# Kernel tuning notes

Measured on AMD Instinct MI355X. Metric: run time of the kernel, lower is better.

Reference implementation:

```python
import jax, jax.numpy as jnp
import numpy as np

B, S, H, I, NH, E = 16, 512, 1024, 4096, 16, 8
DH = H // NH
EPS = 1e-12


def layer_norm(x, g, b):
    mu = jnp.mean(x, axis=-1, keepdims=True)
    var = jnp.mean(jnp.square(x - mu), axis=-1, keepdims=True)
    return (x - mu) * jax.lax.rsqrt(var + EPS) * g + b


def setup_inputs() -> dict:
    key = jax.random.key(0)
    ks = jax.random.split(key, 16)
    s_h = 1.0 / np.sqrt(H)
    s_i = 1.0 / np.sqrt(I)
    return {
        "hidden_states": jax.random.normal(ks[0], (B, S, H), jnp.float32),
        "Wq": jax.random.normal(ks[1], (H, H), jnp.float32) * s_h,
        "bq": jnp.zeros((H,), jnp.float32),
        "Wk": jax.random.normal(ks[2], (H, H), jnp.float32) * s_h,
        "bk": jnp.zeros((H,), jnp.float32),
        "Wv": jax.random.normal(ks[3], (H, H), jnp.float32) * s_h,
        "bv": jnp.zeros((H,), jnp.float32),
        "Wo": jax.random.normal(ks[4], (H, H), jnp.float32) * s_h,
        "bo": jnp.zeros((H,), jnp.float32),
        "ln1_g": jnp.ones((H,), jnp.float32),
        "ln1_b": jnp.zeros((H,), jnp.float32),
        "ln2_g": jnp.ones((H,), jnp.float32),
        "ln2_b": jnp.zeros((H,), jnp.float32),
        "gate_W": jax.random.normal(ks[5], (H, E), jnp.float32) * s_h,
        "W_up": jax.random.normal(ks[6], (E, H, I), jnp.float32) * s_h,
        "b_up": jnp.zeros((E, I), jnp.float32),
        "W_down": jax.random.normal(ks[7], (E, I, H), jnp.float32) * s_i,
        "b_down": jnp.zeros((E, H), jnp.float32),
    }


def reference(hidden_states, Wq, bq, Wk, bk, Wv, bv, Wo, bo,
              ln1_g, ln1_b, ln2_g, ln2_b, gate_W, W_up, b_up, W_down, b_down):
    x = hidden_states
    # --- BERT self-attention ---
    q = (x @ Wq + bq).reshape(B, S, NH, DH)
    k = (x @ Wk + bk).reshape(B, S, NH, DH)
    v = (x @ Wv + bv).reshape(B, S, NH, DH)
    scores = jnp.einsum("bqhd,bkhd->bhqk", q, k) / np.sqrt(DH)
    probs = jax.nn.softmax(scores, axis=-1)
    ctx = jnp.einsum("bhqk,bkhd->bqhd", probs, v).reshape(B, S, H)
    # BertSelfOutput: dense + residual + LayerNorm
    attn_out = layer_norm(ctx @ Wo + bo + x, ln1_g, ln1_b)

    # --- feed_forward_chunk: pre-LN, MoE, residual (residual on attn_out) ---
    x_ln = layer_norm(attn_out, ln2_g, ln2_b)
    router_output = jnp.einsum("bsh,he->bse", x_ln, gate_W)
    router_logits = jnp.mean(router_output, axis=1)          # [B, E]
    choice = jnp.argmax(router_logits, axis=-1)              # softmax-argmax == logits-argmax

    # per-sample top-1 expert: gather each sample's expert weights, batched GEMM
    Wu = W_up[choice]                                        # [B, H, I]
    Wd = W_down[choice]                                      # [B, I, H]
    h = jax.nn.gelu(jnp.einsum("bsh,bhi->bsi", x_ln, Wu) + b_up[choice][:, None, :],
                    approximate=False)
    moe = jnp.einsum("bsi,bih->bsh", h, Wd) + b_down[choice][:, None, :]
    layer_output = moe + attn_out
    return (layer_output, router_logits)
```

## Files before the change

### kernel.cpp

```cpp
#include <hip/hip_runtime.h>


typedef __attribute__((ext_vector_type(4))) float f32x4;
typedef __attribute__((ext_vector_type(8))) short s8v;
typedef __attribute__((ext_vector_type(4))) short s4v;
typedef unsigned short u16;

#define DEV static __device__ __forceinline__

DEV u16 f2bf(float f){
  union { float f; unsigned u; } v; v.f = f;
  unsigned r = v.u + 0x7fffu + ((v.u >> 16) & 1u);
  return (u16)(r >> 16);
}

DEV f32x4 mfma16(s8v a, s8v b, f32x4 c){
  return __builtin_amdgcn_mfma_f32_16x16x32_bf16(a, b, c, 0, 0, 0);
}

DEV float wave_sum(float s){
#pragma unroll
  for (int o = 1; o < 64; o <<= 1) s += __shfl_xor(s, o);
  return s;
}

#define ASYNC_COPY16(g, l) \
  __builtin_amdgcn_global_load_lds((const __attribute__((address_space(1))) void*)(g), \
                                   (__attribute__((address_space(3))) void*)(l), 16, 0, 0)

__global__ __launch_bounds__(256) void cvt_bf16(const float* __restrict__ in,
                                                u16* __restrict__ out)
{
  const size_t i = ((size_t)blockIdx.x * 256 + threadIdx.x) * 8;
  f32x4 a = *(const f32x4*)&in[i];
  f32x4 b = *(const f32x4*)&in[i + 4];
  s8v o;
#pragma unroll
  for (int j = 0; j < 4; ++j){ o[j] = (short)f2bf(a[j]); o[4 + j] = (short)f2bf(b[j]); }
  *(s8v*)&out[i] = o;
}

__global__ __launch_bounds__(256) void transpose_w(const float* __restrict__ in,
                                                   u16* __restrict__ out, int R, int C)
{
  __shared__ float t[64][65];
  const size_t bs = (size_t)blockIdx.z * R * (size_t)C;
  in += bs; out += bs;
  const int c0 = blockIdx.x * 64, r0 = blockIdx.y * 64;
  const int tx = threadIdx.x & 63, ty = threadIdx.x >> 6;
#pragma unroll
  for (int j = 0; j < 64; j += 4) t[ty + j][tx] = in[(size_t)(r0 + ty + j) * C + c0 + tx];
  __syncthreads();
#pragma unroll
  for (int j = 0; j < 64; j += 4) out[(size_t)(c0 + ty + j) * R + r0 + tx] = f2bf(t[tx][ty + j]);
}

template<int MODE, bool SWZ>
__global__ __launch_bounds__(256, 2) void gemm_bt(
    const u16* __restrict__ A, const u16* __restrict__ Bt,
    const float* __restrict__ bias, void* __restrict__ outp,
    const float* __restrict__ resid, int M, int N, int K,
    const int* __restrict__ choice,
    long aBatch, long outBatch, long residBatch, long btExpert, long biasExpert,
    void* __restrict__ out2, void* __restrict__ out3)
{
  int bx, by, bz;
  if (SWZ){
    const int nx = gridDim.x, ny = gridDim.y;
    const int nwg = nx * ny * gridDim.z;
    int id = blockIdx.x + nx * (blockIdx.y + ny * blockIdx.z);
    if ((nwg & 7) == 0){ const int q = nwg >> 3; id = (id & 7) * q + (id >> 3); }
    bx = id % nx; const int r2 = id / nx; by = r2 % ny; bz = r2 / ny;
  } else {
    bx = blockIdx.x; by = blockIdx.y; bz = blockIdx.z;
  }
  const int z = bz;
  if (choice){
    const int e = choice[z];
    Bt   += (size_t)e * btExpert;
    bias += (size_t)e * biasExpert;
  }
  A += (size_t)z * aBatch;

  const int tid = threadIdx.x;
  const int lane = tid & 63, wid = tid >> 6;
  const int hi = lane >> 4, l15 = lane & 15;
  const int wr = wid >> 1, wc = wid & 1;
  const long row0 = (long)bx * 128;
  const long col0 = (long)by * 128;

  __shared__ __align__(16) u16 lA[3][128 * 32];
  __shared__ __align__(16) u16 lB[3][128 * 32];

  f32x4 acc[4][4];
#pragma unroll
  for (int i = 0; i < 4; ++i)
#pragma unroll
    for (int j = 0; j < 4; ++j) acc[i][j] = f32x4{0.f, 0.f, 0.f, 0.f};

  const int r0 = tid >> 2;
  const int scol = (((tid & 3) ^ ((tid >> 3) & 3)) << 3);
  const u16* pA[2]; const u16* pB[2];
#pragma unroll
  for (int j = 0; j < 2; ++j){
    pA[j] = A  + (row0 + j * 64 + r0) * (size_t)K + scol;
    pB[j] = Bt + (col0 + j * 64 + r0) * (size_t)K + scol;
  }

#define GSTAGE(S_) do { \
  _Pragma("unroll") \
  for (int j = 0; j < 2; ++j) ASYNC_COPY16(pA[j], &lA[S_][(j * 256 + tid) * 8]); \
  _Pragma("unroll") \
  for (int j = 0; j < 2; ++j) ASYNC_COPY16(pB[j], &lB[S_][(j * 256 + tid) * 8]); \
  _Pragma("unroll") \
  for (int j = 0; j < 2; ++j){ pA[j] += 32; pB[j] += 32; } \
} while (0)

  const int rkey = (l15 >> 1) & 3;
  const int baseA = (wr * 64 + l15) * 32 + ((hi ^ rkey) << 3);
  const int baseB = (wc * 64 + l15) * 32 + ((hi ^ rkey) << 3);

#define ITER(S_, S2_, WSTR_, DOSTAGE_) do { \
  asm volatile("s_waitcnt vmcnt(" WSTR_ ")" ::: "memory"); \
  __builtin_amdgcn_s_barrier(); \
  __builtin_amdgcn_sched_barrier(0); \
  if (DOSTAGE_) GSTAGE(S2_); \
  s8v af[4], bfv[4]; \
  _Pragma("unroll") \
  for (int mi = 0; mi < 4; ++mi) af[mi] = *(const s8v*)&lA[S_][baseA + mi * 512]; \
  _Pragma("unroll") \
  for (int ni = 0; ni < 4; ++ni) bfv[ni] = *(const s8v*)&lB[S_][baseB + ni * 512]; \
  __builtin_amdgcn_s_setprio(1); \
  _Pragma("unroll") \
  for (int mi = 0; mi < 4; ++mi) \
    _Pragma("unroll") \
    for (int ni = 0; ni < 4; ++ni) \
      acc[mi][ni] = mfma16(af[mi], bfv[ni], acc[mi][ni]); \
  __builtin_amdgcn_s_setprio(0); \
} while (0)

  const int nk = K >> 5;
  GSTAGE(0); GSTAGE(1);

  for (int t = 0; t < nk - 2; t += 3){
    ITER(0, 2, "4", 1);
    ITER(1, 0, "4", 1);
    ITER(2, 1, "4", 1);
  }
  ITER(0, 0, "4", 0);
  ITER(1, 0, "0", 0);
#undef ITER
#undef GSTAGE

#pragma unroll
  for (int mi = 0; mi < 4; ++mi){
    const long rowb = row0 + wr * 64 + mi * 16 + hi * 4;
#pragma unroll
    for (int ni = 0; ni < 4; ++ni){
      const long col = col0 + wc * 64 + ni * 16 + l15;
      const float bv = bias[col];
#pragma unroll
      for (int r = 0; r < 4; ++r){
        const long row = rowb + r;
        float v = acc[mi][ni][r] + bv;
        if (MODE == 2){
          float* o = (float*)outp + (size_t)z * outBatch;
          const float* rs = resid + (size_t)z * residBatch;
          o[row * N + col] = v + rs[row * N + col];
        } else if (MODE == 1){
          u16* o = (u16*)outp + (size_t)z * outBatch;
          const float gv = 0.5f * v * (1.0f + erff(v * 0.70710678118654752f));
          o[row * N + col] = f2bf(gv);
        } else if (MODE == 4){
          const int seg = (int)(col >> 10), lc = (int)(col & 1023);
          const u16 bv16 = f2bf(v);
          if (seg == 0)      ((u16*)outp)[row * 1024 + lc] = bv16;
          else if (seg == 1) ((u16*)out2)[row * 1024 + lc] = bv16;
          else {
            const int bb = (int)(row >> 9), ss = (int)(row & 511);
            const int hh = lc >> 6, dd = lc & 63;
            ((u16*)out3)[(((size_t)(bb * 16 + hh)) * 64 + dd) * 512 + ss] = bv16;
          }
        }
      }
    }
  }
}

__global__ __launch_bounds__(256) void attn_fwd(
    const u16* __restrict__ qb, const u16* __restrict__ kb,
    const u16* __restrict__ vt, u16* __restrict__ ctx)
{
  const int tid = threadIdx.x;
  const int lane = tid & 63, wid = tid >> 6;
  const int hi = lane >> 4, l15 = lane & 15;
  const int h = blockIdx.y, b = blockIdx.z;
  const int q0 = blockIdx.x * 128 + wid * 32;

  const u16* kp0 = kb + (size_t)b * 512 * 1024 + h * 64;
  const u16* vp0 = vt + ((size_t)(b * 16 + h)) * 64 * 512;

  __shared__ __align__(16) u16 lK[2][64 * 64];
  __shared__ __align__(16) u16 lV[2][64 * 64];
  __shared__ __align__(16) u16 lP[4][2][16][72];

#define STAGE(bsel, k0s) do { \
  _Pragma("unroll") \
  for (int i = 0; i < 2; ++i){ \
    const int idx = i * 256 + tid; \
    const int row = idx >> 3, seg = idx & 7; \
    const int sc = ((seg ^ (row & 7)) << 3); \
    ASYNC_COPY16(kp0 + (size_t)((k0s) + row) * 1024 + sc, &lK[bsel][idx * 8]); \
    ASYNC_COPY16(vp0 + (size_t)row * 512 + (k0s) + sc,    &lV[bsel][idx * 8]); \
  } \
} while (0)

  const u16* qp = qb + ((size_t)b * 512 + q0) * 1024 + h * 64;
  s8v qf[2][2];
#pragma unroll
  for (int qt = 0; qt < 2; ++qt)
#pragma unroll
    for (int st = 0; st < 2; ++st)
      qf[qt][st] = *(const s8v*)&qp[(size_t)(qt * 16 + l15) * 1024 + st * 32 + hi * 8];

  f32x4 o[2][4];
#pragma unroll
  for (int qt = 0; qt < 2; ++qt)
#pragma unroll
    for (int mi = 0; mi < 4; ++mi) o[qt][mi] = f32x4{0.f, 0.f, 0.f, 0.f};
  float mrun[2] = {-3e38f, -3e38f}, lrun[2] = {0.f, 0.f};

  STAGE(0, 0);
  __syncthreads();

  for (int t = 0; t < 8; ++t){
    const int buf = t & 1;
    if (t < 7) STAGE(buf ^ 1, (t + 1) * 64);

    f32x4 s[2][4];
#pragma unroll
    for (int qt = 0; qt < 2; ++qt)
#pragma unroll
      for (int kt = 0; kt < 4; ++kt) s[qt][kt] = f32x4{0.f, 0.f, 0.f, 0.f};
#pragma unroll
    for (int st = 0; st < 2; ++st){
      s8v kf[4];
#pragma unroll
      for (int kt = 0; kt < 4; ++kt){
        const int row = kt * 16 + l15;
        kf[kt] = *(const s8v*)&lK[buf][row * 64 + (((st * 4 + hi) ^ (row & 7)) << 3)];
      }
#pragma unroll
      for (int qt = 0; qt < 2; ++qt)
#pragma unroll
        for (int kt = 0; kt < 4; ++kt)
          s[qt][kt] = mfma16(kf[kt], qf[qt][st], s[qt][kt]);
    }

#pragma unroll
    for (int qt = 0; qt < 2; ++qt){
      float mx = s[qt][0][0];
#pragma unroll
      for (int kt = 0; kt < 4; ++kt)
#pragma unroll
        for (int r = 0; r < 4; ++r) mx = fmaxf(mx, s[qt][kt][r]);
      mx *= 0.125f;
      mx = fmaxf(mx, __shfl_xor(mx, 16));
      mx = fmaxf(mx, __shfl_xor(mx, 32));
      const float mnew = fmaxf(mrun[qt], mx);
      const float alpha = __expf(mrun[qt] - mnew);
      mrun[qt] = mnew;
      float ps = 0.f;
#pragma unroll
      for (int kt = 0; kt < 4; ++kt){
        s4v pk;
#pragma unroll
        for (int r = 0; r < 4; ++r){
          const float p = __expf(s[qt][kt][r] * 0.125f - mnew);
          ps += p; pk[r] = (short)f2bf(p);
        }
        *(s4v*)&lP[wid][qt][l15][kt * 16 + 4 * hi] = pk;
      }
      ps += __shfl_xor(ps, 16);
      ps += __shfl_xor(ps, 32);
      lrun[qt] = lrun[qt] * alpha + ps;
#pragma unroll
      for (int mi = 0; mi < 4; ++mi)
#pragma unroll
        for (int r = 0; r < 4; ++r) o[qt][mi][r] *= alpha;
    }

#pragma unroll
    for (int ks = 0; ks < 2; ++ks){
      s8v vf[4];
#pragma unroll
      for (int mi = 0; mi < 4; ++mi){
        const int row = mi * 16 + l15;
        vf[mi] = *(const s8v*)&lV[buf][row * 64 + (((ks * 4 + hi) ^ (row & 7)) << 3)];
      }
#pragma unroll
      for (int qt = 0; qt < 2; ++qt){
        const s8v pf = *(const s8v*)&lP[wid][qt][l15][ks * 32 + 8 * hi];
#pragma unroll
        for (int mi = 0; mi < 4; ++mi)
          o[qt][mi] = mfma16(vf[mi], pf, o[qt][mi]);
      }
    }
    __syncthreads();
  }
#undef STAGE

#pragma unroll
  for (int qt = 0; qt < 2; ++qt){
    const float inv = 1.f / lrun[qt];
    u16* cp = ctx + ((size_t)b * 512 + q0 + qt * 16 + l15) * 1024 + h * 64;
#pragma unroll
    for (int mi = 0; mi < 4; ++mi)
#pragma unroll
      for (int r = 0; r < 4; ++r)
        cp[mi * 16 + 4 * hi + r] = f2bf(o[qt][mi][r] * inv);
  }
}

__global__ __launch_bounds__(256, 2) void ln12_colsum(
    float* __restrict__ t, const float* __restrict__ g1, const float* __restrict__ b1,
    const float* __restrict__ g2, const float* __restrict__ b2,
    u16* __restrict__ xln, float* __restrict__ colsum)
{
  const int b = blockIdx.y;
  const int wid = threadIdx.x >> 6, lane = threadIdx.x & 63;
  __shared__ float cacc[1024];
  for (int i = threadIdx.x; i < 1024; i += 256) cacc[i] = 0.f;
  __syncthreads();
  float acc[16];
#pragma unroll
  for (int i = 0; i < 16; ++i) acc[i] = 0.f;
  const int rbase = b * 512 + blockIdx.x * 64 + wid * 16;
  for (int rr = 0; rr < 16; ++rr){
    float* p = t + (size_t)(rbase + rr) * 1024;
    f32x4 v[4];
#pragma unroll
    for (int c = 0; c < 4; ++c) v[c] = *(const f32x4*)&p[c * 256 + lane * 4];
    float s = 0.f;
#pragma unroll
    for (int c = 0; c < 4; ++c) s += v[c][0] + v[c][1] + v[c][2] + v[c][3];
    const float mu = wave_sum(s) * (1.f / 1024.f);
    float s2 = 0.f;
#pragma unroll
    for (int c = 0; c < 4; ++c)
#pragma unroll
      for (int j = 0; j < 4; ++j){ const float d = v[c][j] - mu; s2 += d * d; }
    const float rs = rsqrtf(wave_sum(s2) * (1.f / 1024.f) + 1e-12f);
    float y1s = 0.f;
#pragma unroll
    for (int c = 0; c < 4; ++c){
      const f32x4 gg = *(const f32x4*)&g1[c * 256 + lane * 4];
      const f32x4 bb = *(const f32x4*)&b1[c * 256 + lane * 4];
#pragma unroll
      for (int j = 0; j < 4; ++j){
        v[c][j] = (v[c][j] - mu) * rs * gg[j] + bb[j];
        y1s += v[c][j];
      }
      *(f32x4*)&p[c * 256 + lane * 4] = v[c];
    }
    const float mu2 = wave_sum(y1s) * (1.f / 1024.f);
    float s22 = 0.f;
#pragma unroll
    for (int c = 0; c < 4; ++c)
#pragma unroll
      for (int j = 0; j < 4; ++j){ const float d = v[c][j] - mu2; s22 += d * d; }
    const float rs2 = rsqrtf(wave_sum(s22) * (1.f / 1024.f) + 1e-12f);
    u16* op = xln + (size_t)(rbase + rr) * 1024;
#pragma unroll
    for (int c = 0; c < 4; ++c){
      const f32x4 gg = *(const f32x4*)&g2[c * 256 + lane * 4];
      const f32x4 bb = *(const f32x4*)&b2[c * 256 + lane * 4];
      s4v ov;
#pragma unroll
      for (int j = 0; j < 4; ++j){
        const float y = (v[c][j] - mu2) * rs2 * gg[j] + bb[j];
        acc[c * 4 + j] += y;
        ov[j] = (short)f2bf(y);
      }
      *(s4v*)&op[c * 256 + lane * 4] = ov;
    }
  }
#pragma unroll
  for (int c = 0; c < 4; ++c)
#pragma unroll
    for (int j = 0; j < 4; ++j)
      atomicAdd(&cacc[c * 256 + lane * 4 + j], acc[c * 4 + j]);
  __syncthreads();
  for (int i = threadIdx.x; i < 1024; i += 256) atomicAdd(&colsum[b * 1024 + i], cacc[i]);
}

__global__ void router_argmax(const float* __restrict__ colsum, const float* __restrict__ gate,
                              float* __restrict__ logits, int* __restrict__ choice)
{
  const int b = blockIdx.x, lane = threadIdx.x;
  float pa[8];
#pragma unroll
  for (int e = 0; e < 8; ++e) pa[e] = 0.f;
  for (int it = 0; it < 16; ++it){
    const int hh = it * 64 + lane;
    const float c = colsum[b * 1024 + hh];
    const float* gp = gate + (size_t)hh * 8;
#pragma unroll
    for (int e = 0; e < 8; ++e) pa[e] += c * gp[e];
  }
#pragma unroll
  for (int e = 0; e < 8; ++e) pa[e] = wave_sum(pa[e]);
  if (lane == 0){
    float best = -3e38f; int bi = 0;
#pragma unroll
    for (int e = 0; e < 8; ++e){
      const float lg = pa[e] * (1.f / 512.f);
      logits[b * 8 + e] = lg;
      if (lg > best){ best = lg; bi = e; }
    }
    choice[b] = bi;
  }
}

extern "C" void kernel_launch(void* const* d_in, const int* in_sizes, int n_in,
                              void* d_out, int out_size, void* d_ws, size_t ws_size,
                              hipStream_t stream)
{
  const float* x    = (const float*)d_in[0];
  const float* Wq   = (const float*)d_in[1];
  const float* bq   = (const float*)d_in[2];
  const float* Wk   = (const float*)d_in[3];
  const float* bk   = (const float*)d_in[4];
  const float* Wv   = (const float*)d_in[5];
  const float* bv   = (const float*)d_in[6];
  const float* Wo   = (const float*)d_in[7];
  const float* bo   = (const float*)d_in[8];
  const float* ln1g = (const float*)d_in[9];
  const float* ln1b = (const float*)d_in[10];
  const float* ln2g = (const float*)d_in[11];
  const float* ln2b = (const float*)d_in[12];
  const float* gate = (const float*)d_in[13];
  const float* Wup  = (const float*)d_in[14];
  const float* bup  = (const float*)d_in[15];
  const float* Wdn  = (const float*)d_in[16];
  const float* bdn  = (const float*)d_in[17];

  size_t off = 0;
  char* wsb = (char*)d_ws;
  auto take = [&](size_t n) -> void* {
    void* p = wsb + off; off += (n + 255) & ~(size_t)255; return p;
  };
  u16*   x_bf  = (u16*)take(8192ull * 1024 * 2);
  u16*   Wqt   = (u16*)take(1024ull * 1024 * 2);
  u16*   Wkt   = (u16*)take(1024ull * 1024 * 2);
  u16*   Wvt   = (u16*)take(1024ull * 1024 * 2);
  u16*   Wot   = (u16*)take(1024ull * 1024 * 2);
  u16*   q_bf  = (u16*)take(8192ull * 1024 * 2);
  u16*   k_bf  = (u16*)take(8192ull * 1024 * 2);
  u16*   vt_bf = (u16*)take(8192ull * 1024 * 2);
  float* tmp   = (float*)take(8192ull * 1024 * 4);
  u16*   Wupt  = (u16*)take(8ull * 4096 * 1024 * 2);
  u16*   Wdnt  = (u16*)take(8ull * 1024 * 4096 * 2);
  u16*   h_bf  = (u16*)take(8192ull * 4096 * 2);
  float* colsum = (float*)take(16ull * 1024 * 4);
  int*   choice = (int*)take(256);
  float* qkvb  = (float*)take(3072 * 4);

  u16* ctx = x_bf;
  u16* xln = q_bf;
  float* logits = (float*)d_out + 8388608;

  cvt_bf16<<<4096, 256, 0, stream>>>(x, x_bf);
  transpose_w<<<dim3(16, 16, 1), 256, 0, stream>>>(Wq,  Wqt,  1024, 1024);
  transpose_w<<<dim3(16, 16, 1), 256, 0, stream>>>(Wk,  Wkt,  1024, 1024);
  transpose_w<<<dim3(16, 16, 1), 256, 0, stream>>>(Wv,  Wvt,  1024, 1024);
  transpose_w<<<dim3(16, 16, 1), 256, 0, stream>>>(Wo,  Wot,  1024, 1024);
  transpose_w<<<dim3(64, 16, 8), 256, 0, stream>>>(Wup, Wupt, 1024, 4096);
  transpose_w<<<dim3(16, 64, 8), 256, 0, stream>>>(Wdn, Wdnt, 4096, 1024);
  hipMemcpyAsync(qkvb,        bq, 1024 * 4, hipMemcpyDeviceToDevice, stream);
  hipMemcpyAsync(qkvb + 1024, bk, 1024 * 4, hipMemcpyDeviceToDevice, stream);
  hipMemcpyAsync(qkvb + 2048, bv, 1024 * 4, hipMemcpyDeviceToDevice, stream);

  gemm_bt<4, true><<<dim3(64, 24, 1), 256, 0, stream>>>(x_bf, Wqt, qkvb, q_bf,
      nullptr, 8192, 3072, 1024, nullptr, 0, 0, 0, 0, 0, k_bf, vt_bf);

  attn_fwd<<<dim3(4, 16, 16), 256, 0, stream>>>(q_bf, k_bf, vt_bf, ctx);

  gemm_bt<2, true><<<dim3(64, 8, 1), 256, 0, stream>>>(ctx, Wot, bo, tmp, x,
      8192, 1024, 1024, nullptr, 0, 0, 0, 0, 0, nullptr, nullptr);
  hipMemsetAsync(colsum, 0, 16 * 1024 * sizeof(float), stream);
  ln12_colsum<<<dim3(8, 16), 256, 0, stream>>>(tmp, ln1g, ln1b, ln2g, ln2b, xln, colsum);
  router_argmax<<<16, 64, 0, stream>>>(colsum, gate, logits, choice);

  gemm_bt<1, true><<<dim3(4, 32, 16), 256, 0, stream>>>(xln, Wupt, bup, h_bf, nullptr,
      512, 4096, 1024, choice, 512ll * 1024, 512ll * 4096, 0, 4096ll * 1024, 4096,
      nullptr, nullptr);
  gemm_bt<2, true><<<dim3(4, 8, 16), 256, 0, stream>>>(h_bf, Wdnt, bdn, d_out, tmp,
      512, 1024, 4096, choice, 512ll * 4096, 512ll * 1024, 512ll * 1024, 1024ll * 4096, 1024,
      nullptr, nullptr);
}
```

Baseline: 551.5 us.

## Deepen GEMM pipeline to four LDS stages with register double-buffered fragments

Moves the GEMM main loop from a 3-stage to a 4-stage LDS ring and double-buffers the MFMA operand fragments in registers. Each iteration now reads the next step's fragments from LDS while issuing MFMAs on the current ones, so LDS latency overlaps with compute and global prefetch runs further ahead. The cost is more LDS per block (64KB instead of 48KB) and more VGPRs for the extra fragment set, which can lower occupancy. The prologue and epilogue iteration sequence now also assumes K/32 is a multiple of 4.

Result: slower. 568.2 us (+3.0%).

```diff
diff --git a/kernel.cpp b/kernel.cpp
--- a/kernel.cpp
+++ b/kernel.cpp
@@ -89,8 +89,8 @@
   const long row0 = (long)bx * 128;
   const long col0 = (long)by * 128;
 
-  __shared__ __align__(16) u16 lA[3][128 * 32];
-  __shared__ __align__(16) u16 lB[3][128 * 32];
+  __shared__ __align__(16) u16 lA[4][128 * 32];
+  __shared__ __align__(16) u16 lB[4][128 * 32];
 
   f32x4 acc[4][4];
 #pragma unroll
@@ -120,36 +120,49 @@
   const int baseA = (wr * 64 + l15) * 32 + ((hi ^ rkey) << 3);
   const int baseB = (wc * 64 + l15) * 32 + ((hi ^ rkey) << 3);
 
-#define ITER(S_, S2_, WSTR_, DOSTAGE_) do { \
-  asm volatile("s_waitcnt vmcnt(" WSTR_ ")" ::: "memory"); \
+  s8v fA[2][4], fB[2][4];
+
+#define LOADFRAGS(P_, S_) do { \
+  _Pragma("unroll") \
+  for (int mi = 0; mi < 4; ++mi) fA[P_][mi] = *(const s8v*)&lA[S_][baseA + mi * 512]; \
+  _Pragma("unroll") \
+  for (int ni = 0; ni < 4; ++ni) fB[P_][ni] = *(const s8v*)&lB[S_][baseB + ni * 512]; \
+} while (0)
+
+#define ITER(VM_, DOSTAGE_, S3_, DOREAD_, S1_, P_) do { \
+  asm volatile("s_waitcnt vmcnt(" VM_ ")" ::: "memory"); \
   __builtin_amdgcn_s_barrier(); \
   __builtin_amdgcn_sched_barrier(0); \
-  if (DOSTAGE_) GSTAGE(S2_); \
-  s8v af[4], bfv[4]; \
-  _Pragma("unroll") \
-  for (int mi = 0; mi < 4; ++mi) af[mi] = *(const s8v*)&lA[S_][baseA + mi * 512]; \
-  _Pragma("unroll") \
-  for (int ni = 0; ni < 4; ++ni) bfv[ni] = *(const s8v*)&lB[S_][baseB + ni * 512]; \
+  if (DOSTAGE_) GSTAGE(S3_); \
+  if (DOREAD_) LOADFRAGS((P_) ^ 1, S1_); \
   __builtin_amdgcn_s_setprio(1); \
   _Pragma("unroll") \
   for (int mi = 0; mi < 4; ++mi) \
     _Pragma("unroll") \
     for (int ni = 0; ni < 4; ++ni) \
-      acc[mi][ni] = mfma16(af[mi], bfv[ni], acc[mi][ni]); \
+      acc[mi][ni] = mfma16(fA[P_][mi], fB[P_][ni], acc[mi][ni]); \
   __builtin_amdgcn_s_setprio(0); \
 } while (0)
 
   const int nk = K >> 5;
-  GSTAGE(0); GSTAGE(1);
-
-  for (int t = 0; t < nk - 2; t += 3){
-    ITER(0, 2, "4", 1);
-    ITER(1, 0, "4", 1);
-    ITER(2, 1, "4", 1);
-  }
-  ITER(0, 0, "4", 0);
-  ITER(1, 0, "0", 0);
+  GSTAGE(0); GSTAGE(1); GSTAGE(2);
+  asm volatile("s_waitcnt vmcnt(8)" ::: "memory");
+  __builtin_amdgcn_s_barrier();
+  __builtin_amdgcn_sched_barrier(0);
+  LOADFRAGS(0, 0);
+
+  for (int t = 0; t < nk - 4; t += 4){
+    ITER("4", 1, 3, 1, 1, 0);
+    ITER("4", 1, 0, 1, 2, 1);
+    ITER("4", 1, 1, 1, 3, 0);
+    ITER("4", 1, 2, 1, 0, 1);
+  }
+  ITER("4", 1, 3, 1, 1, 0);
+  ITER("4", 0, 0, 1, 2, 1);
+  ITER("0", 0, 0, 1, 3, 0);
+  ITER("0", 0, 0, 0, 0, 1);
 #undef ITER
+#undef LOADFRAGS
 #undef GSTAGE
 
 #pragma unroll
```

## Switch GEMM to double-buffered LDS and raise occupancy launch bound

Applied to the files above, without the earlier changes.

Changes the GEMM main loop from a three-stage LDS ring with explicit vmcnt waits and priority hints to a simpler two-stage ping-pong loop with a __syncthreads per K step. The launch bound goes from 2 to 4 blocks per CU, and LDS use per block shrinks. The aim is more resident waves to hide latency. In exchange, the barrier each step likely waits for the prefetch before the next step, which cuts load/compute overlap. The tighter register budget may also cause spills of the 64-float accumulator.

Measured after the change: 549.6 us. Within noise of the previous version (-0.3%).

```diff
diff --git a/kernel.cpp b/kernel.cpp
--- a/kernel.cpp
+++ b/kernel.cpp
@@ -56,7 +56,7 @@
 }
 
 template<int MODE, bool SWZ>
-__global__ __launch_bounds__(256, 2) void gemm_bt(
+__global__ __launch_bounds__(256, 4) void gemm_bt(
     const u16* __restrict__ A, const u16* __restrict__ Bt,
     const float* __restrict__ bias, void* __restrict__ outp,
     const float* __restrict__ resid, int M, int N, int K,
@@ -89,8 +89,8 @@
   const long row0 = (long)bx * 128;
   const long col0 = (long)by * 128;
 
-  __shared__ __align__(16) u16 lA[3][128 * 32];
-  __shared__ __align__(16) u16 lB[3][128 * 32];
+  __shared__ __align__(16) u16 lA[2][128 * 32];
+  __shared__ __align__(16) u16 lB[2][128 * 32];
 
   f32x4 acc[4][4];
 #pragma unroll
@@ -120,36 +120,28 @@
   const int baseA = (wr * 64 + l15) * 32 + ((hi ^ rkey) << 3);
   const int baseB = (wc * 64 + l15) * 32 + ((hi ^ rkey) << 3);
 
-#define ITER(S_, S2_, WSTR_, DOSTAGE_) do { \
-  asm volatile("s_waitcnt vmcnt(" WSTR_ ")" ::: "memory"); \
-  __builtin_amdgcn_s_barrier(); \
-  __builtin_amdgcn_sched_barrier(0); \
-  if (DOSTAGE_) GSTAGE(S2_); \
-  s8v af[4], bfv[4]; \
-  _Pragma("unroll") \
-  for (int mi = 0; mi < 4; ++mi) af[mi] = *(const s8v*)&lA[S_][baseA + mi * 512]; \
-  _Pragma("unroll") \
-  for (int ni = 0; ni < 4; ++ni) bfv[ni] = *(const s8v*)&lB[S_][baseB + ni * 512]; \
-  __builtin_amdgcn_s_setprio(1); \
-  _Pragma("unroll") \
-  for (int mi = 0; mi < 4; ++mi) \
-    _Pragma("unroll") \
-    for (int ni = 0; ni < 4; ++ni) \
-      acc[mi][ni] = mfma16(af[mi], bfv[ni], acc[mi][ni]); \
-  __builtin_amdgcn_s_setprio(0); \
-} while (0)
-
   const int nk = K >> 5;
-  GSTAGE(0); GSTAGE(1);
-
-  for (int t = 0; t < nk - 2; t += 3){
-    ITER(0, 2, "4", 1);
-    ITER(1, 0, "4", 1);
-    ITER(2, 1, "4", 1);
-  }
-  ITER(0, 0, "4", 0);
-  ITER(1, 0, "0", 0);
-#undef ITER
+  GSTAGE(0);
+  __syncthreads();
+
+  for (int t = 0; t < nk; ++t){
+    const int cur = t & 1;
+    if (t + 1 < nk) GSTAGE(cur ^ 1);
+
+    s8v af[4], bfv[4];
+#pragma unroll
+    for (int mi = 0; mi < 4; ++mi)
+      af[mi] = *(const s8v*)&lA[cur][baseA + mi * 512];
+#pragma unroll
+    for (int ni = 0; ni < 4; ++ni)
+      bfv[ni] = *(const s8v*)&lB[cur][baseB + ni * 512];
+#pragma unroll
+    for (int mi = 0; mi < 4; ++mi)
+#pragma unroll
+      for (int ni = 0; ni < 4; ++ni)
+        acc[mi][ni] = mfma16(af[mi], bfv[ni], acc[mi][ni]);
+    __syncthreads();
+  }
 #undef GSTAGE
 
 #pragma unroll
```
